# Kernel optimization log

Hardware: AMD Instinct MI355X
Metric: run time of the kernel (lower is better)

The kernel has to match this reference:

```python
import jax, jax.numpy as jnp
import numpy as np

B, S, D, V = 64, 16, 2048, 128000


def setup_inputs() -> dict:
    key = jax.random.key(0)
    k1, k2, k3, k4, k5 = jax.random.split(key, 5)
    embedding = jax.random.normal(k1, (V, D), dtype=jnp.float32) * 0.02
    hidden_states = jax.random.normal(k2, (B, S, D), dtype=jnp.float32)
    output_positions = jnp.array([S - 1], dtype=jnp.int32)  # sample from last position
    temperatures = jax.random.uniform(k3, (B,), dtype=jnp.float32, minval=0.5, maxval=1.5)
    top_ps = jax.random.uniform(k4, (B,), dtype=jnp.float32, minval=0.7, maxval=1.0)
    top_ks = jax.random.randint(k5, (B,), 1, 64).astype(jnp.int32)
    return {
        "embedding": embedding,
        "hidden_states": hidden_states,
        "output_positions": output_positions,
        "temperatures": temperatures,
        "top_ps": top_ps,
        "top_ks": top_ks,
    }


def reference(embedding, hidden_states, output_positions, temperatures, top_ps, top_ks):
    # select output position: [B, S, D] -> [B, D]
    hs = jnp.take(hidden_states, output_positions, axis=1)[:, 0, :]
    # vocab logits: [B, V]
    logits = jnp.einsum("bd,vd->bv", hs, embedding)
    logits = logits / temperatures[:, None]
    probs = jax.nn.softmax(logits.astype(jnp.float32), axis=-1)
    # descending sort of probs
    order = jnp.argsort(-probs, axis=-1)                       # [B, V]
    probs_sort = jnp.take_along_axis(probs, order, axis=-1)    # [B, V] descending
    cum = jnp.cumsum(probs_sort, axis=-1)
    # top-p: zero everything whose exclusive-prefix mass exceeds top_p
    probs_sort = jnp.where((cum - probs_sort) > top_ps[:, None], 0.0, probs_sort)
    # top-k: keep only first top_k sorted entries
    ranks = jnp.arange(V, dtype=jnp.int32)[None, :]
    probs_sort = jnp.where(ranks >= top_ks[:, None], 0.0, probs_sort)
    # renormalize
    probs_sort = probs_sort / jnp.sum(probs_sort, axis=-1, keepdims=True)
    # scatter back to original vocab order via inverse permutation
    inv = jnp.argsort(order, axis=-1)
    probs_final = jnp.take_along_axis(probs_sort, inv, axis=-1)
    # multinomial sampling (one token per row); zeros -> log 0 = -inf, excluded
    skey = jax.random.key(42)
    next_token_ids = jax.random.categorical(skey, jnp.log(probs_final), axis=-1)
    return next_token_ids
```

## Files before the change

### kernel.cpp

```cpp
#include <hip/hip_runtime.h>
#include <math.h>

#define BATCH 64
#define SEQ 16
#define DIM 2048
#define VOCAB 128000

#define BM 64
#define BN 256
#define BK 32
#define NT (DIM / BK)
#define ASZ (BM * BK)
#define BSZ (BN * BK)
#define NXCD 8

typedef __attribute__((ext_vector_type(8))) short bf16x8;
typedef __attribute__((ext_vector_type(4))) float f32x4;

__device__ __forceinline__ unsigned cvt_pk_bf16(float a, float b) {
  unsigned r;
  asm("v_cvt_pk_bf16_f32 %0, %1, %2" : "=v"(r) : "v"(a), "v"(b));
  return r;
}

__device__ __forceinline__ void split8(float4 x0, float4 x1, bf16x8* hi, bf16x8* lo) {
  float f[8] = {x0.x, x0.y, x0.z, x0.w, x1.x, x1.y, x1.z, x1.w};
  union { unsigned u[4]; bf16x8 v; } H, L;
#pragma unroll
  for (int w = 0; w < 4; ++w) {
    float a = f[2 * w], b = f[2 * w + 1];
    unsigned hp = cvt_pk_bf16(a, b);
    float ha = __uint_as_float(hp << 16);
    float hb = __uint_as_float(hp & 0xffff0000u);
    H.u[w] = hp;
    L.u[w] = cvt_pk_bf16(a - ha, b - hb);
  }
  *hi = H.v;
  *lo = L.v;
}

__device__ __forceinline__ void gload_lds16(const float* src, float* lds_dst) {
  __builtin_amdgcn_global_load_lds(
      (const __attribute__((address_space(1))) void*)src,
      (__attribute__((address_space(3))) void*)lds_dst, 16, 0, 0);
}

__global__ __launch_bounds__(256, 2) void logits_kernel(
    const float* __restrict__ emb,
    const float* __restrict__ hs,
    const int* __restrict__ pos,
    const float* __restrict__ temps,
    float* __restrict__ logits) {
  __shared__ float ldsA[2 * ASZ];
  __shared__ float ldsB[2 * BSZ];

  const int tid = threadIdx.x;
  const int lane = tid & 63;
  const int wid = tid >> 6;
  const int lrow = lane & 15;
  const int lkb = lane >> 4;
  const int p = pos[0];

  const int nwg = VOCAB / BN;
  const int q_ = nwg / NXCD, r_ = nwg % NXCD;
  const int xcd = blockIdx.x % NXCD, idx_ = blockIdx.x / NXCD;
  const int blk = (xcd < r_ ? xcd * (q_ + 1) : r_ * (q_ + 1) + (xcd - r_) * q_) + idx_;
  const int vb = blk * BN + wid * 64;

  const int r8 = (lane >> 3) & 7;
  const int c8 = lane & 7;
  const int cswz = 4 * (c8 ^ r8);

  const float* aSrc[2];
  float* aDst[2];
#pragma unroll
  for (int q = 0; q < 2; ++q) {
    const int g = wid * 2 + q;
    aSrc[q] = hs + ((size_t)(g * 8 + r8) * SEQ + p) * DIM + cswz;
    aDst[q] = &ldsA[g * 8 * BK];
  }
  const float* bSrc[8];
  float* bDst[8];
#pragma unroll
  for (int q = 0; q < 8; ++q) {
    const int g = wid * 8 + q;
    bSrc[q] = emb + (size_t)(blk * BN + g * 8 + r8) * DIM + cswz;
    bDst[q] = &ldsB[g * 8 * BK];
  }

  f32x4 acc[4][4];
#pragma unroll
  for (int i = 0; i < 4; ++i)
#pragma unroll
    for (int j = 0; j < 4; ++j) acc[i][j] = (f32x4){0.f, 0.f, 0.f, 0.f};

  const int sfr = 4 * (lrow & 7);
  const int off0 = (lkb * 8) ^ sfr;
  const int off1 = off0 ^ 4;

#define STAGE(T, BUF)                                                        \
  do {                                                                       \
    const int kof_ = (T) * BK;                                               \
    const int ao_ = (BUF) * ASZ;                                             \
    const int bo_ = (BUF) * BSZ;                                             \
    _Pragma("unroll")                                                        \
    for (int q = 0; q < 2; ++q) gload_lds16(aSrc[q] + kof_, aDst[q] + ao_);  \
    _Pragma("unroll")                                                        \
    for (int q = 0; q < 8; ++q) gload_lds16(bSrc[q] + kof_, bDst[q] + bo_);  \
  } while (0)

  STAGE(0, 0);
  STAGE(1, 1);

  for (int t = 0; t < NT; ++t) {
    const int cur = t & 1;
    if (t < NT - 1) {
      asm volatile("s_waitcnt vmcnt(10)" ::: "memory");
    } else {
      asm volatile("s_waitcnt vmcnt(0)" ::: "memory");
    }
    __builtin_amdgcn_sched_barrier(0);
    __builtin_amdgcn_s_barrier();

    const float* A = &ldsA[cur * ASZ];
    const float* B = &ldsB[cur * BSZ];
    float4 ra[4][2], rb[4][2];
#pragma unroll
    for (int i = 0; i < 4; ++i) {
      const float* rbase = &A[(16 * i + lrow) * BK];
      ra[i][0] = *(const float4*)(rbase + off0);
      ra[i][1] = *(const float4*)(rbase + off1);
    }
#pragma unroll
    for (int j = 0; j < 4; ++j) {
      const float* rbase = &B[(wid * 64 + 16 * j + lrow) * BK];
      rb[j][0] = *(const float4*)(rbase + off0);
      rb[j][1] = *(const float4*)(rbase + off1);
    }
    asm volatile("s_waitcnt lgkmcnt(0)" ::: "memory");
    __builtin_amdgcn_sched_barrier(0);
    __builtin_amdgcn_s_barrier();

    if (t + 2 < NT) STAGE(t + 2, cur);

    bf16x8 ah[4], al[4], bh[4], bl[4];
#pragma unroll
    for (int i = 0; i < 4; ++i) split8(ra[i][0], ra[i][1], &ah[i], &al[i]);
#pragma unroll
    for (int j = 0; j < 4; ++j) split8(rb[j][0], rb[j][1], &bh[j], &bl[j]);
#pragma unroll
    for (int i = 0; i < 4; ++i)
#pragma unroll
      for (int j = 0; j < 4; ++j) {
        acc[i][j] = __builtin_amdgcn_mfma_f32_16x16x32_bf16(ah[i], bh[j], acc[i][j], 0, 0, 0);
        acc[i][j] = __builtin_amdgcn_mfma_f32_16x16x32_bf16(ah[i], bl[j], acc[i][j], 0, 0, 0);
        acc[i][j] = __builtin_amdgcn_mfma_f32_16x16x32_bf16(al[i], bh[j], acc[i][j], 0, 0, 0);
      }
  }
#undef STAGE

#pragma unroll
  for (int i = 0; i < 4; ++i)
#pragma unroll
    for (int r = 0; r < 4; ++r) {
      const int b = 16 * i + lkb * 4 + r;
      const float tt = temps[b];
#pragma unroll
      for (int j = 0; j < 4; ++j) {
        const int v = vb + 16 * j + lrow;
        logits[(size_t)b * VOCAB + v] = acc[i][j][r] / tt;
      }
    }
}

__device__ __forceinline__ void threefry2x32(unsigned k0, unsigned k1,
                                             unsigned x0, unsigned x1,
                                             unsigned* o0, unsigned* o1) {
  const unsigned k2 = k0 ^ k1 ^ 0x1BD11BDAu;
  const unsigned ks[3] = {k0, k1, k2};
  const int rotA[4] = {13, 15, 26, 6};
  const int rotB[4] = {17, 29, 16, 24};
  x0 += k0;
  x1 += k1;
#pragma unroll
  for (int i = 0; i < 5; ++i) {
    const int* rr = (i & 1) ? rotB : rotA;
#pragma unroll
    for (int q = 0; q < 4; ++q) {
      x0 += x1;
      x1 = (x1 << rr[q]) | (x1 >> (32 - rr[q]));
      x1 ^= x0;
    }
    x0 += ks[(i + 1) % 3];
    x1 += ks[(i + 2) % 3] + (unsigned)(i + 1);
  }
  *o0 = x0;
  *o1 = x1;
}

__device__ float gumbel_noise(unsigned flat) {
  unsigned o0, o1;
  threefry2x32(0u, 42u, 0u, flat, &o0, &o1);
  unsigned bits = o0 ^ o1;
  unsigned fb = (bits >> 9) | 0x3f800000u;
  float u = __uint_as_float(fb) - 1.0f;
  const float tiny = 1.17549435e-38f;
  u = fmaxf(u, tiny);
  return -logf(-logf(u));
}

#define CAP 4096
#define NL 12
#define NTH 1024
#define NWAVE 16

__device__ __forceinline__ unsigned sortkey(float x) {
  unsigned bits = __float_as_uint(x);
  return (bits & 0x80000000u) ? ~bits : (bits | 0x80000000u);
}
__device__ __forceinline__ float inv_sortkey(unsigned u) {
  unsigned bits = (u & 0x80000000u) ? (u & 0x7fffffffu) : ~u;
  return __uint_as_float(bits);
}

__global__ __launch_bounds__(NTH) void sample_kernel(
    const float* __restrict__ logits,
    const float* __restrict__ top_ps,
    const int* __restrict__ top_ks,
    const float* __restrict__ temps,
    const int* __restrict__ pos,
    int ws_ok,
    int* __restrict__ out) {
  const int b = blockIdx.x;
  const int tid = threadIdx.x;
  const int lane = tid & 63;
  const int wave = tid >> 6;
  const float* row = logits + (size_t)b * VOCAB;
  const float4* row4 = (const float4*)row;
  const int N4 = VOCAB / 4;

  __shared__ float sred[NWAVE];
  __shared__ int scnt_sh[NL];
  __shared__ float smax, sz;
  __shared__ float sdelta;
  __shared__ unsigned scnt;
  __shared__ unsigned ubuf[CAP];
  __shared__ unsigned ibuf[CAP];
  __shared__ unsigned sorted_u[64];
  __shared__ unsigned sorted_i[64];

  const float D[NL] = {0.5f, 0.75f, 1.0f, 1.25f, 1.5f, 1.75f,
                       2.0f, 2.5f, 3.0f, 4.0f, 8.0f, 1e30f};

  float lmax = -__builtin_huge_valf();
  for (int i = tid; i < N4; i += NTH) {
    float4 v = row4[i];
    lmax = fmaxf(fmaxf(lmax, v.x), fmaxf(fmaxf(v.y, v.z), v.w));
  }
#pragma unroll
  for (int s = 32; s > 0; s >>= 1) lmax = fmaxf(lmax, __shfl_xor(lmax, s, 64));
  if (lane == 0) sred[wave] = lmax;
  if (tid < NL) scnt_sh[tid] = 0;
  __syncthreads();
  if (tid == 0) {
    float m = sred[0];
#pragma unroll
    for (int w = 1; w < NWAVE; ++w) m = fmaxf(m, sred[w]);
    smax = m;
  }
  __syncthreads();
  const float maxl = smax;

  float zsum = 0.f;
  int cnt[NL];
#pragma unroll
  for (int r = 0; r < NL; ++r) cnt[r] = 0;
  for (int i = tid; i < N4; i += NTH) {
    float4 v = row4[i];
    float xs[4] = {v.x, v.y, v.z, v.w};
#pragma unroll
    for (int c = 0; c < 4; ++c) {
      float x = xs[c];
      zsum += expf(x - maxl);
      float d = maxl - x;
#pragma unroll
      for (int r = 0; r < NL; ++r) cnt[r] += (d <= D[r]) ? 1 : 0;
    }
  }
#pragma unroll
  for (int s = 32; s > 0; s >>= 1) {
    zsum += __shfl_xor(zsum, s, 64);
#pragma unroll
    for (int r = 0; r < NL; ++r) cnt[r] += __shfl_xor(cnt[r], s, 64);
  }
  if (lane == 0) {
    sred[wave] = zsum;
#pragma unroll
    for (int r = 0; r < NL; ++r) atomicAdd(&scnt_sh[r], cnt[r]);
  }
  __syncthreads();
  if (tid == 0) {
    float z = 0.f;
#pragma unroll
    for (int w = 0; w < NWAVE; ++w) z += sred[w];
    sz = z;
    float dd = 1e30f;
#pragma unroll
    for (int r = NL - 1; r >= 0; --r)
      if (scnt_sh[r] >= 64) dd = D[r];
    sdelta = dd;
    scnt = 0;
  }
  __syncthreads();
  const float Z = sz;
  const float thrv = maxl - sdelta;

  for (int i = tid; i < N4; i += NTH) {
    float4 v = row4[i];
    float xs[4] = {v.x, v.y, v.z, v.w};
#pragma unroll
    for (int c = 0; c < 4; ++c) {
      if (xs[c] >= thrv) {
        unsigned slot = atomicAdd(&scnt, 1u);
        if (slot < CAP) {
          ubuf[slot] = sortkey(xs[c]);
          ibuf[slot] = (unsigned)(i * 4 + c);
        }
      }
    }
  }
  __syncthreads();
  const int n = (int)(scnt < (unsigned)CAP ? scnt : (unsigned)CAP);

  if (tid < 64) { sorted_u[tid] = 0u; sorted_i[tid] = 0u; }
  __syncthreads();
  for (int c = tid; c < n; c += NTH) {
    unsigned u = ubuf[c], idx = ibuf[c];
    int rank = 0;
    for (int j = 0; j < n; ++j) {
      unsigned uj = ubuf[j];
      rank += (uj > u) || (uj == u && ibuf[j] < idx);
    }
    if (rank < 64) { sorted_u[rank] = u; sorted_i[rank] = idx; }
  }
  __syncthreads();

  if (tid == 0) {
    const float topp = top_ps[b];
    const int k = top_ks[b];
    const float tval = temps[b];
    float cum = 0.f;
    float best = -__builtin_huge_valf();
    int bestidx = 0;
    for (int r = 0; r < 64 && r < n; ++r) {
      float x = inv_sortkey(sorted_u[r]);
      float pr = expf(x - maxl) / Z;
      cum += pr;
      bool keep = (r < k) && !((cum - pr) > topp) && (pr > 0.f);
      if (keep) {
        float g = gumbel_noise((unsigned)b * (unsigned)VOCAB + sorted_i[r]);
        float sc = x + g;
        if (sc > best) { best = sc; bestidx = (int)sorted_i[r]; }
      }
    }
    int token = bestidx;

    unsigned kat0, kat1;
    threefry2x32(0u, 0u, 0u, 0u, &kat0, &kat1);
    bool inputs_ok = (pos[0] >= 0 && pos[0] < SEQ) &&
                     (tval > 0.45f && tval < 1.55f) &&
                     (topp > 0.65f && topp <= 1.0f) &&
                     (k >= 1 && k < 64);
    if (!inputs_ok) token = 3333333;
    else if (!ws_ok) token = 7777777;
    else if (kat0 != 0x6b200159u || kat1 != 0x99ba4efeu) token = 5555555;
    else if (scnt > (unsigned)CAP || n < 64) token = 4444444;
    out[b] = token;
  }
}

extern "C" void kernel_launch(void* const* d_in, const int* in_sizes, int n_in,
                              void* d_out, int out_size, void* d_ws, size_t ws_size,
                              hipStream_t stream) {
  const float* emb   = (const float*)d_in[0];
  const float* hs    = (const float*)d_in[1];
  const int*   pos   = (const int*)d_in[2];
  const float* temps = (const float*)d_in[3];
  const float* topps = (const float*)d_in[4];
  const int*   topks = (const int*)d_in[5];
  float* logits = (float*)d_ws;
  int* out = (int*)d_out;

  const size_t need = (size_t)BATCH * VOCAB * sizeof(float);
  const int ws_ok = (ws_size >= need) ? 1 : 0;

  hipLaunchKernelGGL(logits_kernel, dim3(VOCAB / BN), dim3(256), 0, stream,
                     emb, hs, pos, temps, logits);
  hipLaunchKernelGGL(sample_kernel, dim3(BATCH), dim3(NTH), 0, stream,
                     logits, topps, topks, temps, pos, ws_ok, out);
}
```

Measured before the change: 329.9 us.

## Stage GEMM tiles through registers instead of direct global-to-LDS loads

```diff
diff --git a/kernel.cpp b/kernel.cpp
--- a/kernel.cpp
+++ b/kernel.cpp
@@ -37,12 +37,6 @@
   }
   *hi = H.v;
   *lo = L.v;
-}
-
-__device__ __forceinline__ void gload_lds16(const float* src, float* lds_dst) {
-  __builtin_amdgcn_global_load_lds(
-      (const __attribute__((address_space(1))) void*)src,
-      (__attribute__((address_space(3))) void*)lds_dst, 16, 0, 0);
 }
 
 __global__ __launch_bounds__(256, 2) void logits_kernel(
@@ -69,23 +63,22 @@
 
   const int r8 = (lane >> 3) & 7;
   const int c8 = lane & 7;
-  const int cswz = 4 * (c8 ^ r8);
 
   const float* aSrc[2];
-  float* aDst[2];
+  float* aDstSw[2];
 #pragma unroll
   for (int q = 0; q < 2; ++q) {
     const int g = wid * 2 + q;
-    aSrc[q] = hs + ((size_t)(g * 8 + r8) * SEQ + p) * DIM + cswz;
-    aDst[q] = &ldsA[g * 8 * BK];
+    aSrc[q] = hs + ((size_t)(g * 8 + r8) * SEQ + p) * DIM + 4 * c8;
+    aDstSw[q] = &ldsA[(g * 8 + r8) * BK + 4 * (c8 ^ r8)];
   }
   const float* bSrc[8];
-  float* bDst[8];
+  float* bDstSw[8];
 #pragma unroll
   for (int q = 0; q < 8; ++q) {
     const int g = wid * 8 + q;
-    bSrc[q] = emb + (size_t)(blk * BN + g * 8 + r8) * DIM + cswz;
-    bDst[q] = &ldsB[g * 8 * BK];
+    bSrc[q] = emb + (size_t)(blk * BN + g * 8 + r8) * DIM + 4 * c8;
+    bDstSw[q] = &ldsB[(g * 8 + r8) * BK + 4 * (c8 ^ r8)];
   }
 
   f32x4 acc[4][4];
@@ -98,27 +91,34 @@
   const int off0 = (lkb * 8) ^ sfr;
   const int off1 = off0 ^ 4;
 
-#define STAGE(T, BUF)                                                        \
-  do {                                                                       \
-    const int kof_ = (T) * BK;                                               \
-    const int ao_ = (BUF) * ASZ;                                             \
-    const int bo_ = (BUF) * BSZ;                                             \
-    _Pragma("unroll")                                                        \
-    for (int q = 0; q < 2; ++q) gload_lds16(aSrc[q] + kof_, aDst[q] + ao_);  \
-    _Pragma("unroll")                                                        \
-    for (int q = 0; q < 8; ++q) gload_lds16(bSrc[q] + kof_, bDst[q] + bo_);  \
+  float4 sa[2], sb[8];
+
+#define LOADR(T)                                                         \
+  do {                                                                   \
+    const int kof_ = (T) * BK;                                           \
+    _Pragma("unroll")                                                    \
+    for (int q = 0; q < 2; ++q) sa[q] = *(const float4*)(aSrc[q] + kof_);\
+    _Pragma("unroll")                                                    \
+    for (int q = 0; q < 8; ++q) sb[q] = *(const float4*)(bSrc[q] + kof_);\
   } while (0)
 
-  STAGE(0, 0);
-  STAGE(1, 1);
+#define WRITES(BUF)                                                      \
+  do {                                                                   \
+    const int ao_ = (BUF) * ASZ;                                         \
+    const int bo_ = (BUF) * BSZ;                                         \
+    _Pragma("unroll")                                                    \
+    for (int q = 0; q < 2; ++q) *(float4*)(aDstSw[q] + ao_) = sa[q];     \
+    _Pragma("unroll")                                                    \
+    for (int q = 0; q < 8; ++q) *(float4*)(bDstSw[q] + bo_) = sb[q];     \
+  } while (0)
+
+  LOADR(0);
 
   for (int t = 0; t < NT; ++t) {
     const int cur = t & 1;
-    if (t < NT - 1) {
-      asm volatile("s_waitcnt vmcnt(10)" ::: "memory");
-    } else {
-      asm volatile("s_waitcnt vmcnt(0)" ::: "memory");
-    }
+    WRITES(cur);
+    if (t + 1 < NT) LOADR(t + 1);
+    asm volatile("s_waitcnt lgkmcnt(0)" ::: "memory");
     __builtin_amdgcn_sched_barrier(0);
     __builtin_amdgcn_s_barrier();
 
@@ -137,12 +137,6 @@
       rb[j][0] = *(const float4*)(rbase + off0);
       rb[j][1] = *(const float4*)(rbase + off1);
     }
-    asm volatile("s_waitcnt lgkmcnt(0)" ::: "memory");
-    __builtin_amdgcn_sched_barrier(0);
-    __builtin_amdgcn_s_barrier();
-
-    if (t + 2 < NT) STAGE(t + 2, cur);
-
     bf16x8 ah[4], al[4], bh[4], bl[4];
 #pragma unroll
     for (int i = 0; i < 4; ++i) split8(ra[i][0], ra[i][1], &ah[i], &al[i]);
@@ -157,7 +151,8 @@
         acc[i][j] = __builtin_amdgcn_mfma_f32_16x16x32_bf16(al[i], bh[j], acc[i][j], 0, 0, 0);
       }
   }
-#undef STAGE
+#undef LOADR
+#undef WRITES
 
 #pragma unroll
   for (int i = 0; i < 4; ++i)
```

Measured after the change: 561.8 us. +70.3%, slower.
